# Kernel optimization log

Hardware: AMD Instinct MI355X
Metric: run time of the kernel (lower is better)

Reference implementation:

```python
import jax, jax.numpy as jnp
import numpy as np

IMG_H = IMG_W = 14
HEADS = 8
HEAD_DIM = 32
INNER = HEADS * HEAD_DIM  # 256
IN_CH = 384
OUT_CH = 768
HIDDEN = 4 * IN_CH  # 1536
SCALE = HEAD_DIM ** -0.5
EPS = 1e-5


def _relative_index(h, w):
    # static numpy computation, identical to the torch buffer
    yy, xx = np.meshgrid(np.arange(h), np.arange(w), indexing='ij')
    coords = np.stack([yy.ravel(), xx.ravel()])            # [2, N]
    rel = coords[:, :, None] - coords[:, None, :]          # [2, N, N]
    rel[0] += h - 1
    rel[1] += w - 1
    rel[0] *= 2 * w - 1
    return (rel[0] + rel[1]).reshape(-1)                   # [N*N]


def _maxpool3s2p1(x):
    # torch MaxPool2d(3, 2, 1): pad with -inf
    return jax.lax.reduce_window(
        x, -jnp.inf, jax.lax.max,
        window_dimensions=(1, 1, 3, 3),
        window_strides=(1, 1, 2, 2),
        padding=((0, 0), (0, 0), (1, 1), (1, 1)))


def _layernorm(x, g, b):
    mu = jnp.mean(x, axis=-1, keepdims=True)
    var = jnp.mean(jnp.square(x - mu), axis=-1, keepdims=True)
    return (x - mu) * jax.lax.rsqrt(var + EPS) * g + b


def setup_inputs() -> dict:
    key = jax.random.key(0)
    ks = jax.random.split(key, 12)
    s = 0.02
    return {
        'x': jax.random.normal(ks[0], (64, IN_CH, 28, 28), jnp.float32),
        'W_qkv': jax.random.normal(ks[1], (IN_CH, 3 * INNER), jnp.float32) * s,
        'bias_table': jax.random.normal(ks[2], ((2 * IMG_H - 1) * (2 * IMG_W - 1), HEADS), jnp.float32) * s,
        'W_out': jax.random.normal(ks[3], (INNER, OUT_CH), jnp.float32) * s,
        'b_out': jnp.zeros((OUT_CH,), jnp.float32),
        'ln1_g': jnp.ones((IN_CH,), jnp.float32),
        'ln1_b': jnp.zeros((IN_CH,), jnp.float32),
        'ln2_g': jnp.ones((OUT_CH,), jnp.float32),
        'ln2_b': jnp.zeros((OUT_CH,), jnp.float32),
        'W_fc1': jax.random.normal(ks[4], (OUT_CH, HIDDEN), jnp.float32) * s,
        'b_fc1': jnp.zeros((HIDDEN,), jnp.float32),
        'W_fc2': jax.random.normal(ks[5], (HIDDEN, OUT_CH), jnp.float32) * s,
        'b_fc2': jnp.zeros((OUT_CH,), jnp.float32),
        'W_proj': jax.random.normal(ks[6], (OUT_CH, IN_CH), jnp.float32) * s,
    }


def reference(x, W_qkv, bias_table, W_out, b_out, ln1_g, ln1_b, ln2_g, ln2_b,
              W_fc1, b_fc1, W_fc2, b_fc2, W_proj):
    B = x.shape[0]
    N = IMG_H * IMG_W
    rel_idx = jnp.asarray(_relative_index(IMG_H, IMG_W))   # [N*N]

    # --- downsample branch ---
    xp = _maxpool3s2p1(x)                                  # [B, Cin, 14, 14]
    proj = jnp.einsum('bchw,oc->bohw', xp, W_proj)         # 1x1 conv, no bias

    # --- attention branch ---
    xa = _maxpool3s2p1(x)                                  # [B, Cin, 14, 14]
    tokens = xa.reshape(B, IN_CH, N).transpose(0, 2, 1)    # [B, N, Cin]
    tokens = _layernorm(tokens, ln1_g, ln1_b)
    qkv = tokens @ W_qkv                                   # [B, N, 3*INNER]
    q, k, v = jnp.split(qkv, 3, axis=-1)
    def heads(t):
        return t.reshape(B, N, HEADS, HEAD_DIM).transpose(0, 2, 1, 3)  # [B,H,N,D]
    q, k, v = heads(q), heads(k), heads(v)
    dots = jnp.einsum('bhid,bhjd->bhij', q, k) * SCALE     # [B,H,N,N]
    bias = bias_table[rel_idx].reshape(N, N, HEADS).transpose(2, 0, 1)  # [H,N,N]
    attn = jax.nn.softmax(dots + bias[None], axis=-1)
    out = jnp.einsum('bhij,bhjd->bhid', attn, v)           # [B,H,N,D]
    out = out.transpose(0, 2, 1, 3).reshape(B, N, INNER)
    out = out @ W_out + b_out                              # [B, N, Cout]
    attn_map = out.transpose(0, 2, 1).reshape(B, OUT_CH, IMG_H, IMG_W)

    h = proj + attn_map                                    # [B, Cout, 14, 14]

    # --- feed-forward branch ---
    t = h.reshape(B, OUT_CH, N).transpose(0, 2, 1)         # [B, N, Cout]
    t = _layernorm(t, ln2_g, ln2_b)
    t = jax.nn.gelu(t @ W_fc1 + b_fc1, approximate=False)
    t = t @ W_fc2 + b_fc2
    ffn = t.transpose(0, 2, 1).reshape(B, OUT_CH, IMG_H, IMG_W)

    return h + ffn
```

## Files before the change

### kernel.cpp

```cpp
#include <hip/hip_runtime.h>
#include <hip/hip_bf16.h>
#include <cmath>

typedef unsigned short ushortT;
typedef unsigned int u32;
typedef __attribute__((ext_vector_type(8))) short short8;
typedef __attribute__((ext_vector_type(4))) float floatx4;

#define IMG 14
#define NTOK 196
#define BATCH 64
#define M_TOT 12544
#define M_HALF 6272
#define INCH 384
#define OUTCH 768
#define HIDDEN 1536
#define HEADS 8
#define HDIM 32
#define SCALE 0.17677669529663687f

__device__ __forceinline__ float b2f(ushortT u) {
    union { u32 i; float f; } v; v.i = ((u32)u) << 16; return v.f;
}
__device__ __forceinline__ ushortT f2b(float f) {
    union { float f; u32 i; } v; v.f = f;
    u32 r = v.i + 0x7FFFu + ((v.i >> 16) & 1u);
    return (ushortT)(r >> 16);
}

__device__ __forceinline__ void async_ld16(const void* g, void* l) {
    __builtin_amdgcn_global_load_lds(
        (const __attribute__((address_space(1))) u32*)g,
        (__attribute__((address_space(3))) u32*)l, 16, 0, 0);
}

__global__ __launch_bounds__(256) void prep_pool(
    const float* __restrict__ Wqkv, const float* __restrict__ Wout,
    const float* __restrict__ Wfc1, const float* __restrict__ Wfc2,
    const float* __restrict__ Wproj, const float* __restrict__ x,
    const float* __restrict__ bias_tb,
    ushortT* __restrict__ oQkv, ushortT* __restrict__ oOut,
    ushortT* __restrict__ oFc1, ushortT* __restrict__ oFc2,
    ushortT* __restrict__ oProj, ushortT* __restrict__ pooled,
    float* __restrict__ bias_exp) {
    __shared__ __align__(16) char lds_raw[26880];
    int blk = blockIdx.x;
    int tid = threadIdx.x;
    if (blk >= 4608) {
        int idx4 = (blk - 4608) * 256 + tid;
        int h = idx4 / 10816;
        int rem = idx4 - h * 10816;
        int i = rem / 52;
        int j0 = (rem - i * 52) * 4;
        float v[4];
        #pragma unroll
        for (int u = 0; u < 4; ++u) {
            int j = j0 + u;
            float val = 0.f;
            if (i < 196 && j < 196) {
                int iy = i / 14, ix = i - iy * 14;
                int jy = j / 14, jx = j - jy * 14;
                val = bias_tb[((iy - jy + 13) * 27 + (ix - jx + 13)) * 8 + h];
            }
            v[u] = val;
        }
        *(float4*)(bias_exp + (size_t)idx4 * 4) = *(const float4*)v;
        return;
    }
    if (blk >= 3072) {
        int pblk = blk - 3072;
        int cg = pblk % 24, b = pblk / 24;
        float* hm = (float*)lds_raw;
        const float* xsrc = x + ((size_t)b * INCH + cg * 16) * 784;
        for (int t = tid; t < 448; t += 256) {
            int c = t / 28, hrow = t - c * 28;
            const float* rp = xsrc + c * 784 + hrow * 28;
            float r[28];
            #pragma unroll
            for (int u = 0; u < 7; ++u)
                *(float4*)(r + u * 4) = *(const float4*)(rp + u * 4);
            float* hr = hm + (size_t)t * 15;
            #pragma unroll
            for (int j = 0; j < 14; ++j) {
                float a = j ? r[2 * j - 1] : r[0];
                hr[j] = fmaxf(fmaxf(a, r[2 * j]), r[2 * j + 1]);
            }
        }
        __syncthreads();
        for (int chunk = tid; chunk < NTOK * 2; chunk += 256) {
            int n = chunk >> 1, q = chunk & 1;
            int hh = n / IMG, ww = n - hh * IMG;
            int ya = hh ? 2 * hh - 1 : 0;
            int y1 = 2 * hh, y2 = 2 * hh + 1;
            ushortT o[8];
            #pragma unroll
            for (int cc = 0; cc < 8; ++cc) {
                const float* base = hm + (size_t)(q * 8 + cc) * 28 * 15 + ww;
                float mv = fmaxf(fmaxf(base[ya * 15], base[y1 * 15]), base[y2 * 15]);
                o[cc] = f2b(mv);
            }
            *(uint4*)(pooled + ((size_t)b * NTOK + n) * INCH + cg * 16 + q * 8) =
                *(const uint4*)o;
        }
        return;
    }
    if (blk >= 2784) {
        int i = ((blk - 2784) * 256 + tid) * 4;
        float4 v = *(const float4*)(Wproj + i);
        ushortT o[4] = { f2b(v.x), f2b(v.y), f2b(v.z), f2b(v.w) };
        *(uint2*)(oProj + i) = *(const uint2*)o;
        return;
    }
    const float* in; ushortT* out; int R, C, tile;
    if (blk < 288)       { in = Wqkv; out = oQkv; R = 384;  C = 768;  tile = blk; }
    else if (blk < 480)  { in = Wout; out = oOut; R = 256;  C = 768;  tile = blk - 288; }
    else if (blk < 1632) { in = Wfc1; out = oFc1; R = 768;  C = 1536; tile = blk - 480; }
    else                 { in = Wfc2; out = oFc2; R = 1536; C = 768;  tile = blk - 1632; }
    int tilesX = C >> 5;
    int bx = (tile % tilesX) * 32, by = (tile / tilesX) * 32;
    ushortT (*t)[33] = (ushortT (*)[33])lds_raw;
    int tx = tid & 31, ty = tid >> 5;
    #pragma unroll
    for (int i = 0; i < 4; ++i) {
        int r = by + ty * 4 + i;
        t[ty * 4 + i][tx] = f2b(in[(size_t)r * C + bx + tx]);
    }
    __syncthreads();
    #pragma unroll
    for (int i = 0; i < 4; ++i) {
        int r = bx + ty * 4 + i;
        out[(size_t)r * R + by + tx] = t[tx][ty * 4 + i];
    }
}

template <int VE>
__global__ __launch_bounds__(256) void ln_kernel(const ushortT* __restrict__ in,
                                                 const float* __restrict__ gw,
                                                 const float* __restrict__ bw,
                                                 ushortT* __restrict__ out) {
    constexpr int C = 192 * VE;
    int wave = threadIdx.x >> 6, lane = threadIdx.x & 63;
    int m = blockIdx.x * 4 + wave;
    const ushortT* row = in + (size_t)m * C;
    float v[3][VE];
    float s = 0.f, q = 0.f;
    #pragma unroll
    for (int seg = 0; seg < 3; ++seg) {
        int idx = seg * 64 * VE + lane * VE;
        ushortT tmp[VE];
        if constexpr (VE == 2) *(u32*)tmp = *(const u32*)(row + idx);
        else                   *(uint2*)tmp = *(const uint2*)(row + idx);
        #pragma unroll
        for (int k = 0; k < VE; ++k) {
            float f = b2f(tmp[k]);
            v[seg][k] = f;
            s += f;
            q += f * f;
        }
    }
    #pragma unroll
    for (int off = 32; off > 0; off >>= 1) {
        s += __shfl_xor(s, off, 64);
        q += __shfl_xor(q, off, 64);
    }
    float mu = s / (float)C;
    float var = q / (float)C - mu * mu;
    float rs = rsqrtf(var + 1e-5f);
    #pragma unroll
    for (int seg = 0; seg < 3; ++seg) {
        int idx = seg * 64 * VE + lane * VE;
        float g[VE], bb[VE];
        if constexpr (VE == 2) {
            *(float2*)g = *(const float2*)(gw + idx);
            *(float2*)bb = *(const float2*)(bw + idx);
        } else {
            *(float4*)g = *(const float4*)(gw + idx);
            *(float4*)bb = *(const float4*)(bw + idx);
        }
        ushortT o[VE];
        #pragma unroll
        for (int k = 0; k < VE; ++k)
            o[k] = f2b((v[seg][k] - mu) * rs * g[k] + bb[k]);
        if constexpr (VE == 2) *(u32*)(out + (size_t)m * C + idx) = *(const u32*)o;
        else                   *(uint2*)(out + (size_t)m * C + idx) = *(const uint2*)o;
    }
}

__global__ __launch_bounds__(256) void attn_kernel(const ushortT* __restrict__ qkv,
                                                   const float* __restrict__ bias_exp,
                                                   ushortT* __restrict__ attn_out) {
    int bh = blockIdx.x;
    int b = bh >> 3, h = bh & 7;
    __shared__ ushortT Vts[32 * 232];
    __shared__ ushortT Ps[4][16 * 232];
    const int tid = threadIdx.x, wave = tid >> 6, lane = tid & 63;

    const ushortT* qg = qkv + (size_t)bh * 6272;
    const ushortT* kg = qkv + (size_t)(512 + bh) * 6272;
    const uint4* v4 = (const uint4*)(qkv + (size_t)(1024 + bh) * 6272);
    for (int t = tid; t < 784; t += 256) {
        int j = t >> 2, d0 = (t & 3) * 8;
        uint4 v = v4[t];
        const ushortT* vs = (const ushortT*)&v;
        #pragma unroll
        for (int u = 0; u < 8; ++u)
            Vts[(d0 + u) * 232 + j] = vs[u];
    }
    for (int t = tid; t < 1152; t += 256) {
        int d = t / 36, j = 196 + t - d * 36;
        Vts[d * 232 + j] = 0;
    }
    for (int t = tid; t < 1536; t += 256) {
        int w = t / 384, rem = t - w * 384;
        int row = rem / 24, j = 208 + rem - (rem / 24) * 24;
        Ps[w][row * 232 + j] = 0;
    }
    __syncthreads();

    const int fr = (lane & 15), fk = (lane >> 4) * 8;
    short8 kf[13];
    #pragma unroll
    for (int nt = 0; nt < 13; ++nt)
        kf[nt] = *(const short8*)(kg + (nt * 16 + fr) * 32 + fk);

    const int i0r = (lane >> 4) * 4;
    const int colL = lane & 15;
    ushortT* Pw = &Ps[wave][0];

    for (int mt = wave; mt < 13; mt += 4) {
        short8 af = *(const short8*)(qg + (mt * 16 + fr) * 32 + fk);
        floatx4 sc[13];
        #pragma unroll
        for (int nt = 0; nt < 13; ++nt)
            sc[nt] = __builtin_amdgcn_mfma_f32_16x16x32_bf16(
                af, kf[nt], (floatx4){0.f, 0.f, 0.f, 0.f}, 0, 0, 0);

        float rsum[4] = {0.f, 0.f, 0.f, 0.f};
        const float* bb = bias_exp + ((size_t)h * 208 + mt * 16 + i0r) * 208 + colL;
        #pragma unroll
        for (int nt = 0; nt < 13; ++nt) {
            #pragma unroll
            for (int r = 0; r < 4; ++r) {
                float bias = bb[r * 208 + nt * 16];
                float p = __expf(sc[nt][r] * SCALE + bias);
                if (nt == 12 && colL >= 4) p = 0.f;
                rsum[r] += p;
                Pw[(i0r + r) * 232 + nt * 16 + colL] = f2b(p);
            }
        }
        #pragma unroll
        for (int off = 1; off < 16; off <<= 1) {
            #pragma unroll
            for (int r = 0; r < 4; ++r) rsum[r] += __shfl_xor(rsum[r], off, 64);
        }

        floatx4 o[2];
        o[0] = (floatx4){0.f, 0.f, 0.f, 0.f};
        o[1] = (floatx4){0.f, 0.f, 0.f, 0.f};
        #pragma unroll
        for (int kt = 0; kt < 7; ++kt) {
            short8 pf = *(const short8*)(Pw + fr * 232 + kt * 32 + fk);
            #pragma unroll
            for (int n2 = 0; n2 < 2; ++n2) {
                short8 vf = *(const short8*)(Vts + (n2 * 16 + fr) * 232 + kt * 32 + fk);
                o[n2] = __builtin_amdgcn_mfma_f32_16x16x32_bf16(pf, vf, o[n2], 0, 0, 0);
            }
        }
        float invl[4];
        #pragma unroll
        for (int r = 0; r < 4; ++r) invl[r] = 1.f / rsum[r];
        #pragma unroll
        for (int n2 = 0; n2 < 2; ++n2) {
            #pragma unroll
            for (int r = 0; r < 4; ++r) {
                int i = mt * 16 + i0r + r;
                if (i < 196)
                    attn_out[((size_t)(b * 196 + i)) * 256 + h * 32 + n2 * 16 + colL] =
                        f2b(o[n2][r] * invl[r]);
            }
        }
    }
}

__device__ __forceinline__ void gemm_core128(
    const ushortT* __restrict__ A, const ushortT* __restrict__ B, int K,
    int tm, int tn, ushortT* As, ushortT* Bs,
    floatx4 (&acc)[4][4], int tid, int wave, int lane) {
    const int fr = lane & 15, fk = (lane >> 4) * 8;
    const int wr = (wave >> 1) * 64, wc = (wave & 1) * 64;
    auto stage = [&](int buf, int k0) {
        const ushortT* Ag = A + (size_t)(tm * 128) * K + k0;
        const ushortT* Bg = B + (size_t)(tn * 128) * K + k0;
        ushortT* Al = As + buf * 4096;
        ushortT* Bl = Bs + buf * 4096;
        #pragma unroll
        for (int i = 0; i < 2; ++i) {
            int c = tid + i * 256;
            async_ld16(Ag + (size_t)(c >> 2) * K + (c & 3) * 8, Al + c * 8);
        }
        #pragma unroll
        for (int i = 0; i < 2; ++i) {
            int c = tid + i * 256;
            async_ld16(Bg + (size_t)(c >> 2) * K + (c & 3) * 8, Bl + c * 8);
        }
    };
    const int nsteps = K >> 5;
    stage(0, 0);
    if (nsteps > 1) stage(1, 32);
    for (int t = 0; t < nsteps; ++t) {
        if (t + 1 < nsteps) asm volatile("s_waitcnt vmcnt(4)" ::: "memory");
        else                asm volatile("s_waitcnt vmcnt(0)" ::: "memory");
        __builtin_amdgcn_s_barrier();
        __builtin_amdgcn_sched_barrier(0);
        if (t + 2 < nsteps) stage((t + 2) % 3, (t + 2) * 32);
        const ushortT* Ab = As + (t % 3) * 4096;
        const ushortT* Bb = Bs + (t % 3) * 4096;
        short8 af[4], bf[4];
        #pragma unroll
        for (int mt = 0; mt < 4; ++mt)
            af[mt] = *(const short8*)(Ab + (wr + mt * 16 + fr) * 32 + fk);
        #pragma unroll
        for (int nt = 0; nt < 4; ++nt)
            bf[nt] = *(const short8*)(Bb + (wc + nt * 16 + fr) * 32 + fk);
        #pragma unroll
        for (int mt = 0; mt < 4; ++mt)
            #pragma unroll
            for (int nt = 0; nt < 4; ++nt)
                acc[mt][nt] = __builtin_amdgcn_mfma_f32_16x16x32_bf16(
                    af[mt], bf[nt], acc[mt][nt], 0, 0, 0);
    }
}

__global__ __launch_bounds__(256) void gemm_qkvproj(
    const ushortT* __restrict__ tln1, const ushortT* __restrict__ wTqkv,
    const ushortT* __restrict__ pooled, const ushortT* __restrict__ wProjB,
    const float* __restrict__ b_out, ushortT* __restrict__ qkvb,
    float* __restrict__ outT) {
    __shared__ ushortT As[3 * 4096];
    __shared__ ushortT Bs[3 * 4096];
    const int tid = threadIdx.x, wave = tid >> 6, lane = tid & 63;
    const int tm = blockIdx.x;
    const int y = blockIdx.y;
    const bool isP = y >= 6;
    const int tn = isP ? y - 6 : y;
    const ushortT* A = isP ? pooled : tln1;
    const ushortT* B = isP ? wProjB : wTqkv;

    floatx4 acc[4][4];
    #pragma unroll
    for (int a = 0; a < 4; ++a)
        #pragma unroll
        for (int c = 0; c < 4; ++c)
            acc[a][c] = (floatx4){0.f, 0.f, 0.f, 0.f};

    gemm_core128(A, B, 384, tm, tn, As, Bs, acc, tid, wave, lane);

    const int wr = (wave >> 1) * 64, wc = (wave & 1) * 64;
    const int nb = tn * 128 + wc + (lane & 15);
    const int mbl = wr + ((lane >> 4) << 2);
    if (!isP) {
        #pragma unroll
        for (int nt = 0; nt < 4; ++nt) {
            int n = nb + nt * 16;
            int reg = n >> 8, head = (n >> 5) & 7, d = n & 31;
            #pragma unroll
            for (int mt = 0; mt < 4; ++mt) {
                #pragma unroll
                for (int r = 0; r < 4; ++r) {
                    int m = tm * 128 + mbl + mt * 16 + r;
                    int bb = m / 196, tok = m - bb * 196;
                    qkvb[((size_t)((reg * 512 + bb * 8 + head) * 196 + tok)) * 32 + d] =
                        f2b(acc[mt][nt][r]);
                }
            }
        }
    } else {
        #pragma unroll
        for (int nt = 0; nt < 4; ++nt) {
            int n = nb + nt * 16;
            float bv = b_out[n];
            #pragma unroll
            for (int mt = 0; mt < 4; ++mt) {
                int m0 = tm * 128 + mbl + mt * 16;
                int bb = m0 / 196, tok = m0 - bb * 196;
                float vv[4];
                #pragma unroll
                for (int r = 0; r < 4; ++r) vv[r] = acc[mt][nt][r] + bv;
                *(float4*)(outT + ((size_t)(bb * 768 + n)) * 196 + tok) =
                    *(const float4*)vv;
            }
        }
    }
}

template <int EPI>
__global__ __launch_bounds__(256) void gemm128p(
    const ushortT* __restrict__ A, const ushortT* __restrict__ B, int K,
    const float* __restrict__ bias, ushortT* __restrict__ outb,
    float* __restrict__ outT, int m_off) {
    __shared__ ushortT As[3 * 4096];
    __shared__ ushortT Bs[3 * 4096];
    const int tid = threadIdx.x, wave = tid >> 6, lane = tid & 63;
    const int tm = blockIdx.x, tn = blockIdx.y;

    floatx4 acc[4][4];
    #pragma unroll
    for (int a = 0; a < 4; ++a)
        #pragma unroll
        for (int c = 0; c < 4; ++c)
            acc[a][c] = (floatx4){0.f, 0.f, 0.f, 0.f};

    gemm_core128(A, B, K, tm, tn, As, Bs, acc, tid, wave, lane);

    const int wr = (wave >> 1) * 64, wc = (wave & 1) * 64;
    const int nb = tn * 128 + wc + (lane & 15);
    const int mbl = wr + ((lane >> 4) << 2);
    #pragma unroll
    for (int nt = 0; nt < 4; ++nt) {
        int n = nb + nt * 16;
        float bv = (EPI == 2 || EPI == 3) ? bias[n] : 0.f;
        #pragma unroll
        for (int mt = 0; mt < 4; ++mt) {
            int m0 = tm * 128 + mbl + mt * 16;
            if constexpr (EPI == 1) {
                int bb = m0 / 196, tok = m0 - bb * 196;
                float* p = outT + ((size_t)(bb * 768 + n)) * 196 + tok;
                float hv[4];
                *(float4*)hv = *(const float4*)p;
                float vv[4];
                #pragma unroll
                for (int r = 0; r < 4; ++r) vv[r] = acc[mt][nt][r] + hv[r];
                *(float4*)p = *(const float4*)vv;
                #pragma unroll
                for (int r = 0; r < 4; ++r)
                    outb[(size_t)(m0 + r) * 768 + n] = f2b(vv[r]);
            } else if constexpr (EPI == 2) {
                #pragma unroll
                for (int r = 0; r < 4; ++r) {
                    float v = acc[mt][nt][r] + bv;
                    float gl = 0.5f * v * (1.f + erff(v * 0.70710678118654752f));
                    outb[(size_t)(m0 + r) * 1536 + n] = f2b(gl);
                }
            } else {
                int mg = m0 + m_off;
                int bb = mg / 196, tok = mg - bb * 196;
                float* p = outT + ((size_t)(bb * 768 + n)) * 196 + tok;
                float hv[4];
                *(float4*)hv = *(const float4*)p;
                float vv[4];
                #pragma unroll
                for (int r = 0; r < 4; ++r) vv[r] = acc[mt][nt][r] + bv + hv[r];
                *(float4*)p = *(const float4*)vv;
            }
        }
    }
}

extern "C" void kernel_launch(void* const* d_in, const int* in_sizes, int n_in,
                              void* d_out, int out_size, void* d_ws, size_t ws_size,
                              hipStream_t stream) {
    const float* x       = (const float*)d_in[0];
    const float* W_qkv   = (const float*)d_in[1];
    const float* bias_tb = (const float*)d_in[2];
    const float* W_out   = (const float*)d_in[3];
    const float* b_out   = (const float*)d_in[4];
    const float* ln1_g   = (const float*)d_in[5];
    const float* ln1_b   = (const float*)d_in[6];
    const float* ln2_g   = (const float*)d_in[7];
    const float* ln2_b   = (const float*)d_in[8];
    const float* W_fc1   = (const float*)d_in[9];
    const float* b_fc1   = (const float*)d_in[10];
    const float* W_fc2   = (const float*)d_in[11];
    const float* b_fc2   = (const float*)d_in[12];
    const float* W_proj  = (const float*)d_in[13];
    float* out = (float*)d_out;

    char* ws = (char*)d_ws;
    ushortT* pooled = (ushortT*)(ws);
    ushortT* tln1   = (ushortT*)(ws + 9633792);
    ushortT* attno  = tln1;
    ushortT* qkvb   = (ushortT*)(ws + 19267584);
    ushortT* tln2   = qkvb;
    ushortT* mid    = (ushortT*)(ws);
    ushortT* htok   = (ushortT*)(ws + 38535168);
    float*   bias_exp = (float*)(ws + 38535168);
    ushortT* wTqkv  = (ushortT*)(ws + 57802752);
    ushortT* wTout  = wTqkv + 768 * 384;
    ushortT* wTfc1  = wTout + 768 * 256;
    ushortT* wTfc2  = wTfc1 + 1536 * 768;
    ushortT* wProjB = wTfc2 + 768 * 1536;
    const size_t weights_end = 57802752 +
        (size_t)(768 * 384 + 768 * 256 + 1536 * 768 + 768 * 1536 + 768 * 384) * 2;
    const bool ffn_full = ws_size >= weights_end + (size_t)M_TOT * HIDDEN * 2;
    ushortT* midf = (ushortT*)(ws + weights_end);

    prep_pool<<<4946, 256, 0, stream>>>(W_qkv, W_out, W_fc1, W_fc2, W_proj, x, bias_tb,
                                        wTqkv, wTout, wTfc1, wTfc2, wProjB, pooled,
                                        bias_exp);

    ln_kernel<2><<<M_TOT / 4, 256, 0, stream>>>(pooled, ln1_g, ln1_b, tln1);

    gemm_qkvproj<<<dim3(98, 12), 256, 0, stream>>>(tln1, wTqkv, pooled, wProjB,
                                                   b_out, qkvb, out);
    attn_kernel<<<512, 256, 0, stream>>>(qkvb, bias_exp, attno);

    gemm128p<1><<<dim3(98, 6), 256, 0, stream>>>(attno, wTout, 256,
                                                 nullptr, htok, out, 0);
    ln_kernel<4><<<M_TOT / 4, 256, 0, stream>>>(htok, ln2_g, ln2_b, tln2);

    if (ffn_full) {
        gemm128p<2><<<dim3(98, 12), 256, 0, stream>>>(tln2, wTfc1, 768,
                                                      b_fc1, midf, nullptr, 0);
        gemm128p<3><<<dim3(98, 6), 256, 0, stream>>>(midf, wTfc2, 1536,
                                                     b_fc2, nullptr, out, 0);
    } else {
        for (int half = 0; half < 2; ++half) {
            const ushortT* a2 = tln2 + (size_t)half * M_HALF * 768;
            gemm128p<2><<<dim3(49, 12), 256, 0, stream>>>(a2, wTfc1, 768,
                                                          b_fc1, mid, nullptr, 0);
            gemm128p<3><<<dim3(49, 6), 256, 0, stream>>>(mid, wTfc2, 1536,
                                                         b_fc2, nullptr, out,
                                                         half * M_HALF);
        }
    }
    (void)in_sizes; (void)n_in; (void)out_size; (void)ws_size;
}
```

Before: 395.0 us.

## Split-K the FC2 GEMM with atomics and switch GEMM core to double buffering

Replaces the FC2 GEMM with a split-K variant that launches two K-halves per tile and accumulates into the fp32 output with atomicAdd, doubling the block count so the 588-block grid fills the GPU better. The shared GEMM core also moves from a 3-stage async pipeline with explicit vmcnt waits to a 2-stage buffer with __syncthreads, which cuts LDS use per block. In exchange the output sees atomic traffic and non-deterministic summation order. The shallower pipeline may expose more load latency in every GEMM.

```diff
diff --git a/kernel.cpp b/kernel.cpp
--- a/kernel.cpp
+++ b/kernel.cpp
@@ -283,38 +283,34 @@
 }
 
 __device__ __forceinline__ void gemm_core128(
-    const ushortT* __restrict__ A, const ushortT* __restrict__ B, int K,
+    const ushortT* __restrict__ A, const ushortT* __restrict__ B,
+    int nsteps, int lda, int ldb,
     int tm, int tn, ushortT* As, ushortT* Bs,
     floatx4 (&acc)[4][4], int tid, int wave, int lane) {
     const int fr = lane & 15, fk = (lane >> 4) * 8;
     const int wr = (wave >> 1) * 64, wc = (wave & 1) * 64;
     auto stage = [&](int buf, int k0) {
-        const ushortT* Ag = A + (size_t)(tm * 128) * K + k0;
-        const ushortT* Bg = B + (size_t)(tn * 128) * K + k0;
+        const ushortT* Ag = A + (size_t)(tm * 128) * lda + k0;
+        const ushortT* Bg = B + (size_t)(tn * 128) * ldb + k0;
         ushortT* Al = As + buf * 4096;
         ushortT* Bl = Bs + buf * 4096;
         #pragma unroll
         for (int i = 0; i < 2; ++i) {
             int c = tid + i * 256;
-            async_ld16(Ag + (size_t)(c >> 2) * K + (c & 3) * 8, Al + c * 8);
+            async_ld16(Ag + (size_t)(c >> 2) * lda + (c & 3) * 8, Al + c * 8);
         }
         #pragma unroll
         for (int i = 0; i < 2; ++i) {
             int c = tid + i * 256;
-            async_ld16(Bg + (size_t)(c >> 2) * K + (c & 3) * 8, Bl + c * 8);
+            async_ld16(Bg + (size_t)(c >> 2) * ldb + (c & 3) * 8, Bl + c * 8);
         }
     };
-    const int nsteps = K >> 5;
     stage(0, 0);
-    if (nsteps > 1) stage(1, 32);
     for (int t = 0; t < nsteps; ++t) {
-        if (t + 1 < nsteps) asm volatile("s_waitcnt vmcnt(4)" ::: "memory");
-        else                asm volatile("s_waitcnt vmcnt(0)" ::: "memory");
-        __builtin_amdgcn_s_barrier();
-        __builtin_amdgcn_sched_barrier(0);
-        if (t + 2 < nsteps) stage((t + 2) % 3, (t + 2) * 32);
-        const ushortT* Ab = As + (t % 3) * 4096;
-        const ushortT* Bb = Bs + (t % 3) * 4096;
+        __syncthreads();
+        if (t + 1 < nsteps) stage((t + 1) & 1, (t + 1) * 32);
+        const ushortT* Ab = As + (t & 1) * 4096;
+        const ushortT* Bb = Bs + (t & 1) * 4096;
         short8 af[4], bf[4];
         #pragma unroll
         for (int mt = 0; mt < 4; ++mt)
@@ -336,8 +332,8 @@
     const ushortT* __restrict__ pooled, const ushortT* __restrict__ wProjB,
     const float* __restrict__ b_out, ushortT* __restrict__ qkvb,
     float* __restrict__ outT) {
-    __shared__ ushortT As[3 * 4096];
-    __shared__ ushortT Bs[3 * 4096];
+    __shared__ ushortT As[2 * 4096];
+    __shared__ ushortT Bs[2 * 4096];
     const int tid = threadIdx.x, wave = tid >> 6, lane = tid & 63;
     const int tm = blockIdx.x;
     const int y = blockIdx.y;
@@ -353,7 +349,7 @@
         for (int c = 0; c < 4; ++c)
             acc[a][c] = (floatx4){0.f, 0.f, 0.f, 0.f};
 
-    gemm_core128(A, B, 384, tm, tn, As, Bs, acc, tid, wave, lane);
+    gemm_core128(A, B, 12, 384, 384, tm, tn, As, Bs, acc, tid, wave, lane);
 
     const int wr = (wave >> 1) * 64, wc = (wave & 1) * 64;
     const int nb = tn * 128 + wc + (lane & 15);
@@ -398,8 +394,8 @@
     const ushortT* __restrict__ A, const ushortT* __restrict__ B, int K,
     const float* __restrict__ bias, ushortT* __restrict__ outb,
     float* __restrict__ outT, int m_off) {
-    __shared__ ushortT As[3 * 4096];
-    __shared__ ushortT Bs[3 * 4096];
+    __shared__ ushortT As[2 * 4096];
+    __shared__ ushortT Bs[2 * 4096];
     const int tid = threadIdx.x, wave = tid >> 6, lane = tid & 63;
     const int tm = blockIdx.x, tn = blockIdx.y;
 
@@ -410,7 +406,7 @@
         for (int c = 0; c < 4; ++c)
             acc[a][c] = (floatx4){0.f, 0.f, 0.f, 0.f};
 
-    gemm_core128(A, B, K, tm, tn, As, Bs, acc, tid, wave, lane);
+    gemm_core128(A, B, K >> 5, K, K, tm, tn, As, Bs, acc, tid, wave, lane);
 
     const int wr = (wave >> 1) * 64, wc = (wave & 1) * 64;
     const int nb = tn * 128 + wc + (lane & 15);
@@ -418,7 +414,7 @@
     #pragma unroll
     for (int nt = 0; nt < 4; ++nt) {
         int n = nb + nt * 16;
-        float bv = (EPI == 2 || EPI == 3) ? bias[n] : 0.f;
+        float bv = (EPI == 2) ? bias[n] : 0.f;
         #pragma unroll
         for (int mt = 0; mt < 4; ++mt) {
             int m0 = tm * 128 + mbl + mt * 16;
@@ -434,24 +430,52 @@
                 #pragma unroll
                 for (int r = 0; r < 4; ++r)
                     outb[(size_t)(m0 + r) * 768 + n] = f2b(vv[r]);
-            } else if constexpr (EPI == 2) {
+            } else {
                 #pragma unroll
                 for (int r = 0; r < 4; ++r) {
                     float v = acc[mt][nt][r] + bv;
                     float gl = 0.5f * v * (1.f + erff(v * 0.70710678118654752f));
                     outb[(size_t)(m0 + r) * 1536 + n] = f2b(gl);
                 }
-            } else {
-                int mg = m0 + m_off;
-                int bb = mg / 196, tok = mg - bb * 196;
-                float* p = outT + ((size_t)(bb * 768 + n)) * 196 + tok;
-                float hv[4];
-                *(float4*)hv = *(const float4*)p;
-                float vv[4];
-                #pragma unroll
-                for (int r = 0; r < 4; ++r) vv[r] = acc[mt][nt][r] + bv + hv[r];
-                *(float4*)p = *(const float4*)vv;
-            }
+            }
+        }
+    }
+}
+
+__global__ __launch_bounds__(256) void gemm_fc2s(
+    const ushortT* __restrict__ A, const ushortT* __restrict__ B,
+    const float* __restrict__ bias, float* __restrict__ outT, int m_off) {
+    __shared__ ushortT As[2 * 4096];
+    __shared__ ushortT Bs[2 * 4096];
+    const int tid = threadIdx.x, wave = tid >> 6, lane = tid & 63;
+    const int tm = blockIdx.x, tn = blockIdx.y, z = blockIdx.z;
+    const ushortT* Az = A + z * 768;
+    const ushortT* Bz = B + z * 768;
+
+    floatx4 acc[4][4];
+    #pragma unroll
+    for (int a = 0; a < 4; ++a)
+        #pragma unroll
+        for (int c = 0; c < 4; ++c)
+            acc[a][c] = (floatx4){0.f, 0.f, 0.f, 0.f};
+
+    gemm_core128(Az, Bz, 24, 1536, 1536, tm, tn, As, Bs, acc, tid, wave, lane);
+
+    const int wr = (wave >> 1) * 64, wc = (wave & 1) * 64;
+    const int nb = tn * 128 + wc + (lane & 15);
+    const int mbl = wr + ((lane >> 4) << 2);
+    #pragma unroll
+    for (int nt = 0; nt < 4; ++nt) {
+        int n = nb + nt * 16;
+        float bv = z ? 0.f : bias[n];
+        #pragma unroll
+        for (int mt = 0; mt < 4; ++mt) {
+            int mg = tm * 128 + mbl + mt * 16 + m_off;
+            int bb = mg / 196, tok = mg - bb * 196;
+            float* p = outT + ((size_t)(bb * 768 + n)) * 196 + tok;
+            #pragma unroll
+            for (int r = 0; r < 4; ++r)
+                atomicAdd(p + r, acc[mt][nt][r] + bv);
         }
     }
 }
@@ -511,16 +535,14 @@
     if (ffn_full) {
         gemm128p<2><<<dim3(98, 12), 256, 0, stream>>>(tln2, wTfc1, 768,
                                                       b_fc1, midf, nullptr, 0);
-        gemm128p<3><<<dim3(98, 6), 256, 0, stream>>>(midf, wTfc2, 1536,
-                                                     b_fc2, nullptr, out, 0);
+        gemm_fc2s<<<dim3(98, 6, 2), 256, 0, stream>>>(midf, wTfc2, b_fc2, out, 0);
     } else {
         for (int half = 0; half < 2; ++half) {
             const ushortT* a2 = tln2 + (size_t)half * M_HALF * 768;
             gemm128p<2><<<dim3(49, 12), 256, 0, stream>>>(a2, wTfc1, 768,
                                                           b_fc1, mid, nullptr, 0);
-            gemm128p<3><<<dim3(49, 6), 256, 0, stream>>>(mid, wTfc2, 1536,
-                                                         b_fc2, nullptr, out,
-                                                         half * M_HALF);
+            gemm_fc2s<<<dim3(49, 6, 2), 256, 0, stream>>>(mid, wTfc2, b_fc2, out,
+                                                          half * M_HALF);
         }
     }
     (void)in_sizes; (void)n_in; (void)out_size; (void)ws_size;
```

Result: slower. 801.4 us (+102.9%).

## Switch GEMM core to double-buffered pipeline with templated K-tile depth

Applied to the files above, without the earlier changes.

Replaces the 3-stage async-copy pipeline (vmcnt waits plus raw barrier) with a simpler 2-buffer scheme that uses __syncthreads and prefetches one tile ahead. The K tile depth becomes a template parameter, and the out-projection and fc2 GEMMs use BK=64 to halve barrier count per K. The aim is less synchronization overhead and LDS use per block. The trade-off is less prefetch depth: the barrier now waits for all outstanding loads, so memory latency may be exposed.

```diff
diff --git a/kernel.cpp b/kernel.cpp
--- a/kernel.cpp
+++ b/kernel.cpp
@@ -282,52 +282,55 @@
     }
 }
 
+template <int BK>
 __device__ __forceinline__ void gemm_core128(
-    const ushortT* __restrict__ A, const ushortT* __restrict__ B, int K,
+    const ushortT* __restrict__ A, const ushortT* __restrict__ B,
+    int nsteps, int lda, int ldb,
     int tm, int tn, ushortT* As, ushortT* Bs,
     floatx4 (&acc)[4][4], int tid, int wave, int lane) {
+    constexpr int TILE = 128 * BK;
+    constexpr int CPT = TILE / 8 / 256;
+    constexpr int CW = BK / 8;
     const int fr = lane & 15, fk = (lane >> 4) * 8;
     const int wr = (wave >> 1) * 64, wc = (wave & 1) * 64;
     auto stage = [&](int buf, int k0) {
-        const ushortT* Ag = A + (size_t)(tm * 128) * K + k0;
-        const ushortT* Bg = B + (size_t)(tn * 128) * K + k0;
-        ushortT* Al = As + buf * 4096;
-        ushortT* Bl = Bs + buf * 4096;
-        #pragma unroll
-        for (int i = 0; i < 2; ++i) {
+        const ushortT* Ag = A + (size_t)(tm * 128) * lda + k0;
+        const ushortT* Bg = B + (size_t)(tn * 128) * ldb + k0;
+        ushortT* Al = As + buf * TILE;
+        ushortT* Bl = Bs + buf * TILE;
+        #pragma unroll
+        for (int i = 0; i < CPT; ++i) {
             int c = tid + i * 256;
-            async_ld16(Ag + (size_t)(c >> 2) * K + (c & 3) * 8, Al + c * 8);
-        }
-        #pragma unroll
-        for (int i = 0; i < 2; ++i) {
+            async_ld16(Ag + (size_t)(c / CW) * lda + (c % CW) * 8, Al + c * 8);
+        }
+        #pragma unroll
+        for (int i = 0; i < CPT; ++i) {
             int c = tid + i * 256;
-            async_ld16(Bg + (size_t)(c >> 2) * K + (c & 3) * 8, Bl + c * 8);
+            async_ld16(Bg + (size_t)(c / CW) * ldb + (c % CW) * 8, Bl + c * 8);
         }
     };
-    const int nsteps = K >> 5;
     stage(0, 0);
-    if (nsteps > 1) stage(1, 32);
     for (int t = 0; t < nsteps; ++t) {
-        if (t + 1 < nsteps) asm volatile("s_waitcnt vmcnt(4)" ::: "memory");
-        else                asm volatile("s_waitcnt vmcnt(0)" ::: "memory");
-        __builtin_amdgcn_s_barrier();
-        __builtin_amdgcn_sched_barrier(0);
-        if (t + 2 < nsteps) stage((t + 2) % 3, (t + 2) * 32);
-        const ushortT* Ab = As + (t % 3) * 4096;
-        const ushortT* Bb = Bs + (t % 3) * 4096;
-        short8 af[4], bf[4];
-        #pragma unroll
-        for (int mt = 0; mt < 4; ++mt)
-            af[mt] = *(const short8*)(Ab + (wr + mt * 16 + fr) * 32 + fk);
-        #pragma unroll
-        for (int nt = 0; nt < 4; ++nt)
-            bf[nt] = *(const short8*)(Bb + (wc + nt * 16 + fr) * 32 + fk);
-        #pragma unroll
-        for (int mt = 0; mt < 4; ++mt)
+        __syncthreads();
+        if (t + 1 < nsteps) stage((t + 1) & 1, (t + 1) * BK);
+        const ushortT* Ab = As + (t & 1) * TILE;
+        const ushortT* Bb = Bs + (t & 1) * TILE;
+        #pragma unroll
+        for (int ks = 0; ks < BK / 32; ++ks) {
+            short8 af[4], bf[4];
+            #pragma unroll
+            for (int mt = 0; mt < 4; ++mt)
+                af[mt] = *(const short8*)(Ab + (wr + mt * 16 + fr) * BK + ks * 32 + fk);
             #pragma unroll
             for (int nt = 0; nt < 4; ++nt)
-                acc[mt][nt] = __builtin_amdgcn_mfma_f32_16x16x32_bf16(
-                    af[mt], bf[nt], acc[mt][nt], 0, 0, 0);
+                bf[nt] = *(const short8*)(Bb + (wc + nt * 16 + fr) * BK + ks * 32 + fk);
+            #pragma unroll
+            for (int mt = 0; mt < 4; ++mt)
+                #pragma unroll
+                for (int nt = 0; nt < 4; ++nt)
+                    acc[mt][nt] = __builtin_amdgcn_mfma_f32_16x16x32_bf16(
+                        af[mt], bf[nt], acc[mt][nt], 0, 0, 0);
+        }
     }
 }
 
@@ -336,8 +339,8 @@
     const ushortT* __restrict__ pooled, const ushortT* __restrict__ wProjB,
     const float* __restrict__ b_out, ushortT* __restrict__ qkvb,
     float* __restrict__ outT) {
-    __shared__ ushortT As[3 * 4096];
-    __shared__ ushortT Bs[3 * 4096];
+    __shared__ ushortT As[2 * 4096];
+    __shared__ ushortT Bs[2 * 4096];
     const int tid = threadIdx.x, wave = tid >> 6, lane = tid & 63;
     const int tm = blockIdx.x;
     const int y = blockIdx.y;
@@ -353,7 +356,7 @@
         for (int c = 0; c < 4; ++c)
             acc[a][c] = (floatx4){0.f, 0.f, 0.f, 0.f};
 
-    gemm_core128(A, B, 384, tm, tn, As, Bs, acc, tid, wave, lane);
+    gemm_core128<32>(A, B, 12, 384, 384, tm, tn, As, Bs, acc, tid, wave, lane);
 
     const int wr = (wave >> 1) * 64, wc = (wave & 1) * 64;
     const int nb = tn * 128 + wc + (lane & 15);
@@ -393,13 +396,13 @@
     }
 }
 
-template <int EPI>
+template <int EPI, int BK>
 __global__ __launch_bounds__(256) void gemm128p(
     const ushortT* __restrict__ A, const ushortT* __restrict__ B, int K,
     const float* __restrict__ bias, ushortT* __restrict__ outb,
     float* __restrict__ outT, int m_off) {
-    __shared__ ushortT As[3 * 4096];
-    __shared__ ushortT Bs[3 * 4096];
+    __shared__ ushortT As[2 * 128 * BK];
+    __shared__ ushortT Bs[2 * 128 * BK];
     const int tid = threadIdx.x, wave = tid >> 6, lane = tid & 63;
     const int tm = blockIdx.x, tn = blockIdx.y;
 
@@ -410,7 +413,7 @@
         for (int c = 0; c < 4; ++c)
             acc[a][c] = (floatx4){0.f, 0.f, 0.f, 0.f};
 
-    gemm_core128(A, B, K, tm, tn, As, Bs, acc, tid, wave, lane);
+    gemm_core128<BK>(A, B, K / BK, K, K, tm, tn, As, Bs, acc, tid, wave, lane);
 
     const int wr = (wave >> 1) * 64, wc = (wave & 1) * 64;
     const int nb = tn * 128 + wc + (lane & 15);
@@ -504,23 +507,23 @@
                                                    b_out, qkvb, out);
     attn_kernel<<<512, 256, 0, stream>>>(qkvb, bias_exp, attno);
 
-    gemm128p<1><<<dim3(98, 6), 256, 0, stream>>>(attno, wTout, 256,
-                                                 nullptr, htok, out, 0);
+    gemm128p<1, 64><<<dim3(98, 6), 256, 0, stream>>>(attno, wTout, 256,
+                                                     nullptr, htok, out, 0);
     ln_kernel<4><<<M_TOT / 4, 256, 0, stream>>>(htok, ln2_g, ln2_b, tln2);
 
     if (ffn_full) {
-        gemm128p<2><<<dim3(98, 12), 256, 0, stream>>>(tln2, wTfc1, 768,
-                                                      b_fc1, midf, nullptr, 0);
-        gemm128p<3><<<dim3(98, 6), 256, 0, stream>>>(midf, wTfc2, 1536,
-                                                     b_fc2, nullptr, out, 0);
+        gemm128p<2, 32><<<dim3(98, 12), 256, 0, stream>>>(tln2, wTfc1, 768,
+                                                          b_fc1, midf, nullptr, 0);
+        gemm128p<3, 64><<<dim3(98, 6), 256, 0, stream>>>(midf, wTfc2, 1536,
+                                                         b_fc2, nullptr, out, 0);
     } else {
         for (int half = 0; half < 2; ++half) {
             const ushortT* a2 = tln2 + (size_t)half * M_HALF * 768;
-            gemm128p<2><<<dim3(49, 12), 256, 0, stream>>>(a2, wTfc1, 768,
-                                                          b_fc1, mid, nullptr, 0);
-            gemm128p<3><<<dim3(49, 6), 256, 0, stream>>>(mid, wTfc2, 1536,
-                                                         b_fc2, nullptr, out,
-                                                         half * M_HALF);
+            gemm128p<2, 32><<<dim3(49, 12), 256, 0, stream>>>(a2, wTfc1, 768,
+                                                              b_fc1, mid, nullptr, 0);
+            gemm128p<3, 64><<<dim3(49, 6), 256, 0, stream>>>(mid, wTfc2, 1536,
+                                                             b_fc2, nullptr, out,
+                                                             half * M_HALF);
         }
     }
     (void)in_sizes; (void)n_in; (void)out_size; (void)ws_size;
```

Result: slower. 425.9 us (+7.8%).

## Template GEMM core on M tile, use 64-row tiles for narrow GEMMs, double-buffer

Applied to the files above, without the earlier changes.

Generalizes the shared GEMM core to a templated M-tile size and launches the out-projection and fc2 GEMMs with 64-row tiles, doubling their block count to better fill the GPU's compute units (98x6 blocks is below a full wave). It also replaces the 3-stage async pipeline with explicit vmcnt waits by a simpler 2-buffer scheme with __syncthreads per K-step, reducing LDS usage. The simpler pipeline may expose more memory latency, and smaller tiles reduce B-operand reuse.

```diff
diff --git a/kernel.cpp b/kernel.cpp
--- a/kernel.cpp
+++ b/kernel.cpp
@@ -282,48 +282,47 @@
     }
 }
 
-__device__ __forceinline__ void gemm_core128(
-    const ushortT* __restrict__ A, const ushortT* __restrict__ B, int K,
-    int tm, int tn, ushortT* As, ushortT* Bs,
-    floatx4 (&acc)[4][4], int tid, int wave, int lane) {
+template <int BM>
+__device__ __forceinline__ void gemm_core(
+    const ushortT* __restrict__ A, const ushortT* __restrict__ B,
+    int nsteps, int lda, int ldb, int tm, int tn,
+    ushortT* As, ushortT* Bs, floatx4 (&acc)[BM / 32][4],
+    int tid, int wave, int lane) {
+    constexpr int MT = BM / 32;
+    constexpr int ATILE = BM * 32;
     const int fr = lane & 15, fk = (lane >> 4) * 8;
-    const int wr = (wave >> 1) * 64, wc = (wave & 1) * 64;
+    const int wr = (wave >> 1) * (BM / 2), wc = (wave & 1) * 64;
     auto stage = [&](int buf, int k0) {
-        const ushortT* Ag = A + (size_t)(tm * 128) * K + k0;
-        const ushortT* Bg = B + (size_t)(tn * 128) * K + k0;
-        ushortT* Al = As + buf * 4096;
+        const ushortT* Ag = A + (size_t)(tm * BM) * lda + k0;
+        const ushortT* Bg = B + (size_t)(tn * 128) * ldb + k0;
+        ushortT* Al = As + buf * ATILE;
         ushortT* Bl = Bs + buf * 4096;
+        #pragma unroll
+        for (int i = 0; i < BM / 64; ++i) {
+            int c = tid + i * 256;
+            async_ld16(Ag + (size_t)(c >> 2) * lda + (c & 3) * 8, Al + c * 8);
+        }
         #pragma unroll
         for (int i = 0; i < 2; ++i) {
             int c = tid + i * 256;
-            async_ld16(Ag + (size_t)(c >> 2) * K + (c & 3) * 8, Al + c * 8);
-        }
-        #pragma unroll
-        for (int i = 0; i < 2; ++i) {
-            int c = tid + i * 256;
-            async_ld16(Bg + (size_t)(c >> 2) * K + (c & 3) * 8, Bl + c * 8);
+            async_ld16(Bg + (size_t)(c >> 2) * ldb + (c & 3) * 8, Bl + c * 8);
         }
     };
-    const int nsteps = K >> 5;
     stage(0, 0);
-    if (nsteps > 1) stage(1, 32);
     for (int t = 0; t < nsteps; ++t) {
-        if (t + 1 < nsteps) asm volatile("s_waitcnt vmcnt(4)" ::: "memory");
-        else                asm volatile("s_waitcnt vmcnt(0)" ::: "memory");
-        __builtin_amdgcn_s_barrier();
-        __builtin_amdgcn_sched_barrier(0);
-        if (t + 2 < nsteps) stage((t + 2) % 3, (t + 2) * 32);
-        const ushortT* Ab = As + (t % 3) * 4096;
-        const ushortT* Bb = Bs + (t % 3) * 4096;
-        short8 af[4], bf[4];
-        #pragma unroll
-        for (int mt = 0; mt < 4; ++mt)
+        __syncthreads();
+        if (t + 1 < nsteps) stage((t + 1) & 1, (t + 1) * 32);
+        const ushortT* Ab = As + (t & 1) * ATILE;
+        const ushortT* Bb = Bs + (t & 1) * 4096;
+        short8 af[MT], bf[4];
+        #pragma unroll
+        for (int mt = 0; mt < MT; ++mt)
             af[mt] = *(const short8*)(Ab + (wr + mt * 16 + fr) * 32 + fk);
         #pragma unroll
         for (int nt = 0; nt < 4; ++nt)
             bf[nt] = *(const short8*)(Bb + (wc + nt * 16 + fr) * 32 + fk);
         #pragma unroll
-        for (int mt = 0; mt < 4; ++mt)
+        for (int mt = 0; mt < MT; ++mt)
             #pragma unroll
             for (int nt = 0; nt < 4; ++nt)
                 acc[mt][nt] = __builtin_amdgcn_mfma_f32_16x16x32_bf16(
@@ -336,8 +335,8 @@
     const ushortT* __restrict__ pooled, const ushortT* __restrict__ wProjB,
     const float* __restrict__ b_out, ushortT* __restrict__ qkvb,
     float* __restrict__ outT) {
-    __shared__ ushortT As[3 * 4096];
-    __shared__ ushortT Bs[3 * 4096];
+    __shared__ ushortT As[2 * 4096];
+    __shared__ ushortT Bs[2 * 4096];
     const int tid = threadIdx.x, wave = tid >> 6, lane = tid & 63;
     const int tm = blockIdx.x;
     const int y = blockIdx.y;
@@ -353,7 +352,7 @@
         for (int c = 0; c < 4; ++c)
             acc[a][c] = (floatx4){0.f, 0.f, 0.f, 0.f};
 
-    gemm_core128(A, B, 384, tm, tn, As, Bs, acc, tid, wave, lane);
+    gemm_core<128>(A, B, 12, 384, 384, tm, tn, As, Bs, acc, tid, wave, lane);
 
     const int wr = (wave >> 1) * 64, wc = (wave & 1) * 64;
     const int nb = tn * 128 + wc + (lane & 15);
@@ -393,26 +392,27 @@
     }
 }
 
-template <int EPI>
+template <int EPI, int BM>
 __global__ __launch_bounds__(256) void gemm128p(
     const ushortT* __restrict__ A, const ushortT* __restrict__ B, int K,
     const float* __restrict__ bias, ushortT* __restrict__ outb,
     float* __restrict__ outT, int m_off) {
-    __shared__ ushortT As[3 * 4096];
-    __shared__ ushortT Bs[3 * 4096];
+    __shared__ ushortT As[2 * BM * 32];
+    __shared__ ushortT Bs[2 * 4096];
     const int tid = threadIdx.x, wave = tid >> 6, lane = tid & 63;
     const int tm = blockIdx.x, tn = blockIdx.y;
-
-    floatx4 acc[4][4];
-    #pragma unroll
-    for (int a = 0; a < 4; ++a)
+    constexpr int MT = BM / 32;
+
+    floatx4 acc[MT][4];
+    #pragma unroll
+    for (int a = 0; a < MT; ++a)
         #pragma unroll
         for (int c = 0; c < 4; ++c)
             acc[a][c] = (floatx4){0.f, 0.f, 0.f, 0.f};
 
-    gemm_core128(A, B, K, tm, tn, As, Bs, acc, tid, wave, lane);
-
-    const int wr = (wave >> 1) * 64, wc = (wave & 1) * 64;
+    gemm_core<BM>(A, B, K >> 5, K, K, tm, tn, As, Bs, acc, tid, wave, lane);
+
+    const int wr = (wave >> 1) * (BM / 2), wc = (wave & 1) * 64;
     const int nb = tn * 128 + wc + (lane & 15);
     const int mbl = wr + ((lane >> 4) << 2);
     #pragma unroll
@@ -420,8 +420,8 @@
         int n = nb + nt * 16;
         float bv = (EPI == 2 || EPI == 3) ? bias[n] : 0.f;
         #pragma unroll
-        for (int mt = 0; mt < 4; ++mt) {
-            int m0 = tm * 128 + mbl + mt * 16;
+        for (int mt = 0; mt < MT; ++mt) {
+            int m0 = tm * BM + mbl + mt * 16;
             if constexpr (EPI == 1) {
                 int bb = m0 / 196, tok = m0 - bb * 196;
                 float* p = outT + ((size_t)(bb * 768 + n)) * 196 + tok;
@@ -504,23 +504,23 @@
                                                    b_out, qkvb, out);
     attn_kernel<<<512, 256, 0, stream>>>(qkvb, bias_exp, attno);
 
-    gemm128p<1><<<dim3(98, 6), 256, 0, stream>>>(attno, wTout, 256,
-                                                 nullptr, htok, out, 0);
+    gemm128p<1, 64><<<dim3(196, 6), 256, 0, stream>>>(attno, wTout, 256,
+                                                      nullptr, htok, out, 0);
     ln_kernel<4><<<M_TOT / 4, 256, 0, stream>>>(htok, ln2_g, ln2_b, tln2);
 
     if (ffn_full) {
-        gemm128p<2><<<dim3(98, 12), 256, 0, stream>>>(tln2, wTfc1, 768,
-                                                      b_fc1, midf, nullptr, 0);
-        gemm128p<3><<<dim3(98, 6), 256, 0, stream>>>(midf, wTfc2, 1536,
-                                                     b_fc2, nullptr, out, 0);
+        gemm128p<2, 128><<<dim3(98, 12), 256, 0, stream>>>(tln2, wTfc1, 768,
+                                                           b_fc1, midf, nullptr, 0);
+        gemm128p<3, 64><<<dim3(196, 6), 256, 0, stream>>>(midf, wTfc2, 1536,
+                                                          b_fc2, nullptr, out, 0);
     } else {
         for (int half = 0; half < 2; ++half) {
             const ushortT* a2 = tln2 + (size_t)half * M_HALF * 768;
-            gemm128p<2><<<dim3(49, 12), 256, 0, stream>>>(a2, wTfc1, 768,
-                                                          b_fc1, mid, nullptr, 0);
-            gemm128p<3><<<dim3(49, 6), 256, 0, stream>>>(mid, wTfc2, 1536,
-                                                         b_fc2, nullptr, out,
-                                                         half * M_HALF);
+            gemm128p<2, 128><<<dim3(49, 12), 256, 0, stream>>>(a2, wTfc1, 768,
+                                                               b_fc1, mid, nullptr, 0);
+            gemm128p<3, 64><<<dim3(98, 6), 256, 0, stream>>>(mid, wTfc2, 1536,
+                                                             b_fc2, nullptr, out,
+                                                             half * M_HALF);
         }
     }
     (void)in_sizes; (void)n_in; (void)out_size; (void)ws_size;
```

After: 408.1 us. +3.3%, slower.
